# Kernel optimization log

Hardware: AMD Instinct MI355X
Metric: run time of the kernel (lower is better)

## Reference

```python
import jax, jax.numpy as jnp
import numpy as np

B, T, DIN, H, DOUT = 256, 512, 128, 256, 64
LEAK = 0.01


def setup_inputs() -> dict:
    key = jax.random.key(0)
    k0, k1, k2, k3, k4, k5, k6 = jax.random.split(key, 7)
    inputs = jax.random.normal(k0, (B, T, DIN), dtype=jnp.float32)
    # original uses torch.rand(...) * sqrt(dim) for initial states
    x0 = jax.random.uniform(k1, (B, DOUT), dtype=jnp.float32) * (DOUT ** 0.5)
    h0 = jax.random.uniform(k2, (B, H), dtype=jnp.float32) * (H ** 0.5)
    # nn.Linear default init scale ~ 1/sqrt(fan_in)
    s1 = (DIN + H) ** -0.5
    s2 = H ** -0.5
    W_ih = jax.random.uniform(k3, (H, DIN + H), dtype=jnp.float32, minval=-s1, maxval=s1)
    b_ih = jax.random.uniform(k4, (H,), dtype=jnp.float32, minval=-s1, maxval=s1)
    W_ho = jax.random.uniform(k5, (DOUT, H), dtype=jnp.float32, minval=-s2, maxval=s2)
    b_ho = jax.random.uniform(k6, (DOUT,), dtype=jnp.float32, minval=-s2, maxval=s2)
    return {"inputs": inputs, "x0": x0, "h0": h0,
            "W_ih": W_ih, "b_ih": b_ih, "W_ho": W_ho, "b_ho": b_ho}


def reference(inputs, x0, h0, W_ih, b_ih, W_ho, b_ho):
    # inputs: [B, T, DIN]; scan over time with hidden state resident.
    def step(h, u_t):  # h: [B,H], u_t: [B,DIN]
        comb = jnp.concatenate([u_t, h], axis=1)           # [B, DIN+H]
        pre = comb @ W_ih.T + b_ih                          # [B, H]
        h_new = jnp.where(pre >= 0, pre, LEAK * pre)        # LeakyReLU(0.01)
        x_t = h_new @ W_ho.T + b_ho                         # [B, DOUT]
        return h_new, (x_t, h_new)

    u_seq = jnp.swapaxes(inputs, 0, 1)                      # [T, B, DIN]
    _, (xs, hs) = jax.lax.scan(step, h0, u_seq)
    # prepend initial states -> [B, T+1, *]
    x = jnp.concatenate([x0[:, None, :], jnp.swapaxes(xs, 0, 1)], axis=1)
    h = jnp.concatenate([h0[:, None, :], jnp.swapaxes(hs, 0, 1)], axis=1)
    return x, h
```

## Files before the change

### kernel.cpp

```cpp
#include <hip/hip_runtime.h>

#define BB 256
#define TT 512
#define DIN 128
#define HH 256
#define DOUT 64
#define X_ELEMS ((long)BB * 513 * DOUT)

typedef short bf16x8 __attribute__((ext_vector_type(8)));
typedef float f32x4 __attribute__((ext_vector_type(4)));
typedef _Float16 half2_t __attribute__((ext_vector_type(2)));
typedef _Float16 half8_t __attribute__((ext_vector_type(8)));

static __device__ inline short f2bf(float f) {
    unsigned u = __float_as_uint(f);
    unsigned r = (u + 0x7FFFu + ((u >> 16) & 1u)) >> 16;
    return (short)r;
}

static __device__ inline float fdot2f(half2_t a, half2_t b, float c) {
#if __has_builtin(__builtin_amdgcn_fdot2)
    return __builtin_amdgcn_fdot2(a, b, c, false);
#else
    return c + (float)a[0] * (float)b[0] + (float)a[1] * (float)b[1];
#endif
}

static __device__ inline float quad_bfly_add(float x) {
    int t = __builtin_amdgcn_mov_dpp(__float_as_int(x), 0xB1, 0xF, 0xF, true);
    x += __int_as_float(t);
    t = __builtin_amdgcn_mov_dpp(__float_as_int(x), 0x4E, 0xF, 0xF, true);
    x += __int_as_float(t);
    return x;
}

#define SA 136
__global__ __launch_bounds__(256) void gemm_u(
        const float* __restrict__ inp, const float* __restrict__ W_ih,
        const float* __restrict__ b_ih, float* __restrict__ out_h) {
    __shared__ __align__(16) short lA[64 * SA];
    __shared__ __align__(16) short lB[64 * SA];
    const int tid = threadIdx.x;
    const int wave = tid >> 6, lane = tid & 63;
    const int quad = lane >> 4, l16 = lane & 15;
    const int m0 = blockIdx.x * 64;
    const int n0 = blockIdx.y * 64;
    const int sm = tid >> 2, skg = tid & 3;
    const int sn = tid & 63, bkg = tid >> 6;

    float4 a4[8], b4[8];
#pragma unroll
    for (int c = 0; c < 4; ++c) {
        const float4* ap = (const float4*)(inp + (long)(m0 + sm) * DIN + c * 32 + skg * 8);
        a4[2 * c] = ap[0]; a4[2 * c + 1] = ap[1];
        const float4* bp = (const float4*)(W_ih + (long)(n0 + sn) * 384 + c * 32 + bkg * 8);
        b4[2 * c] = bp[0]; b4[2 * c + 1] = bp[1];
    }
#pragma unroll
    for (int c = 0; c < 4; ++c) {
        bf16x8 av, bv;
        float4 x0 = a4[2 * c], x1 = a4[2 * c + 1];
        av[0] = f2bf(x0.x); av[1] = f2bf(x0.y); av[2] = f2bf(x0.z); av[3] = f2bf(x0.w);
        av[4] = f2bf(x1.x); av[5] = f2bf(x1.y); av[6] = f2bf(x1.z); av[7] = f2bf(x1.w);
        float4 y0 = b4[2 * c], y1 = b4[2 * c + 1];
        bv[0] = f2bf(y0.x); bv[1] = f2bf(y0.y); bv[2] = f2bf(y0.z); bv[3] = f2bf(y0.w);
        bv[4] = f2bf(y1.x); bv[5] = f2bf(y1.y); bv[6] = f2bf(y1.z); bv[7] = f2bf(y1.w);
        *(bf16x8*)&lA[sm * SA + c * 32 + skg * 8] = av;
        *(bf16x8*)&lB[sn * SA + c * 32 + bkg * 8] = bv;
    }
    __syncthreads();

    f32x4 acc[4];
#pragma unroll
    for (int i = 0; i < 4; i++) acc[i] = (f32x4){0.f, 0.f, 0.f, 0.f};
#pragma unroll
    for (int c = 0; c < 4; ++c) {
        bf16x8 af = *(const bf16x8*)&lA[(wave * 16 + l16) * SA + c * 32 + quad * 8];
#pragma unroll
        for (int nt = 0; nt < 4; ++nt) {
            bf16x8 bf = *(const bf16x8*)&lB[(nt * 16 + l16) * SA + c * 32 + quad * 8];
            acc[nt] = __builtin_amdgcn_mfma_f32_16x16x32_bf16(af, bf, acc[nt], 0, 0, 0);
        }
    }
#pragma unroll
    for (int nt = 0; nt < 4; ++nt) {
#pragma unroll
        for (int r = 0; r < 4; ++r) {
            int m = m0 + wave * 16 + quad * 4 + r;
            int col = n0 + nt * 16 + l16;
            long orow = (long)(m >> 9) * 513 + (m & 511) + 1;
            out_h[orow * HH + col] = acc[nt][r] + b_ih[col];
        }
    }
}

__global__ __launch_bounds__(256) void rnn_seq(
        const float* __restrict__ x0, const float* __restrict__ h0,
        const float* __restrict__ W_ih,
        float* __restrict__ out_x, float* __restrict__ out_h) {
    __shared__ __align__(16) _Float16 hsh[2][4][72];
    const int b = blockIdx.x;
    const int tid = threadIdx.x;
    const int g = tid >> 2;
    const int q = tid & 3;
    const int jm = (g << 2) + q;

    half2_t w[4][32];
    {
        const float* base = W_ih + 128 + 64 * q;
#pragma unroll
        for (int jp = 0; jp < 4; ++jp) {
            const float* wr = base + (long)(4 * g + jp) * 384;
#pragma unroll
            for (int i = 0; i < 16; ++i) {
                float4 v = *(const float4*)(wr + 4 * i);
                w[jp][2 * i]     = (half2_t){(_Float16)v.x, (_Float16)v.y};
                w[jp][2 * i + 1] = (half2_t){(_Float16)v.z, (_Float16)v.w};
            }
        }
    }

    float* hrow = out_h + (long)b * 513 * HH;
    {
        float hv = h0[(long)b * HH + jm];
        hrow[jm] = hv;
        hsh[0][jm >> 6][jm & 63] = (_Float16)hv;
    }
    if (tid < DOUT) out_x[(long)b * 513 * DOUT + tid] = x0[(long)b * DOUT + tid];
    float u = hrow[HH + jm];
    __syncthreads();

    int cur = 0;
    for (int t = 0; t < TT; ++t) {
        const _Float16* hs = &hsh[cur][q][0];
        float a0 = 0.f, a1 = 0.f, a2 = 0.f, a3 = 0.f;
#pragma unroll
        for (int c = 0; c < 8; ++c) {
            half8_t hv = *(const half8_t*)(hs + 8 * c);
            half2_t p0 = {hv[0], hv[1]}, p1 = {hv[2], hv[3]};
            half2_t p2 = {hv[4], hv[5]}, p3 = {hv[6], hv[7]};
            a0 = fdot2f(p0, w[0][4 * c + 0], a0);
            a0 = fdot2f(p1, w[0][4 * c + 1], a0);
            a0 = fdot2f(p2, w[0][4 * c + 2], a0);
            a0 = fdot2f(p3, w[0][4 * c + 3], a0);
            a1 = fdot2f(p0, w[1][4 * c + 0], a1);
            a1 = fdot2f(p1, w[1][4 * c + 1], a1);
            a1 = fdot2f(p2, w[1][4 * c + 2], a1);
            a1 = fdot2f(p3, w[1][4 * c + 3], a1);
            a2 = fdot2f(p0, w[2][4 * c + 0], a2);
            a2 = fdot2f(p1, w[2][4 * c + 1], a2);
            a2 = fdot2f(p2, w[2][4 * c + 2], a2);
            a2 = fdot2f(p3, w[2][4 * c + 3], a2);
            a3 = fdot2f(p0, w[3][4 * c + 0], a3);
            a3 = fdot2f(p1, w[3][4 * c + 1], a3);
            a3 = fdot2f(p2, w[3][4 * c + 2], a3);
            a3 = fdot2f(p3, w[3][4 * c + 3], a3);
        }
        a0 = quad_bfly_add(a0);
        a1 = quad_bfly_add(a1);
        a2 = quad_bfly_add(a2);
        a3 = quad_bfly_add(a3);
        float s = (q == 0) ? a0 : (q == 1) ? a1 : (q == 2) ? a2 : a3;
        float tot = s + u;
        float hn = tot >= 0.f ? tot : 0.01f * tot;
        int nxt = cur ^ 1;
        hsh[nxt][jm >> 6][jm & 63] = (_Float16)hn;
        hrow[(long)(t + 1) * HH + jm] = hn;
        if (t < TT - 1) u = hrow[(long)(t + 2) * HH + jm];
        __syncthreads();
        cur = nxt;
    }
}

#define SX 264
__global__ __launch_bounds__(256) void gemm_x(
        const float* __restrict__ out_h, const float* __restrict__ W_ho,
        const float* __restrict__ b_ho, float* __restrict__ out_x) {
    __shared__ __align__(16) short lA[64 * SX];
    __shared__ __align__(16) short lB[64 * SX];
    const int tid = threadIdx.x;
    const int wave = tid >> 6, lane = tid & 63;
    const int quad = lane >> 4, l16 = lane & 15;
    const int m0 = blockIdx.x * 64;
    const int bb = m0 >> 9, t0 = m0 & 511;
    const float* hsrc = out_h + ((long)bb * 513 + 1 + t0) * HH;
    float* xdst = out_x + ((long)bb * 513 + 1 + t0) * DOUT;
    const int sm = tid >> 2, skg = tid & 3;
    const int sn = tid & 63, bkg = tid >> 6;

#pragma unroll
    for (int ph = 0; ph < 2; ++ph) {
        float4 a4[8], b4[8];
#pragma unroll
        for (int c = 0; c < 4; ++c) {
            int k0 = ph * 128 + c * 32;
            const float4* ap = (const float4*)(hsrc + (long)sm * HH + k0 + skg * 8);
            a4[2 * c] = ap[0]; a4[2 * c + 1] = ap[1];
            const float4* bp = (const float4*)(W_ho + (long)sn * HH + k0 + bkg * 8);
            b4[2 * c] = bp[0]; b4[2 * c + 1] = bp[1];
        }
#pragma unroll
        for (int c = 0; c < 4; ++c) {
            int k0 = ph * 128 + c * 32;
            bf16x8 av, bv;
            float4 x0 = a4[2 * c], x1 = a4[2 * c + 1];
            av[0] = f2bf(x0.x); av[1] = f2bf(x0.y); av[2] = f2bf(x0.z); av[3] = f2bf(x0.w);
            av[4] = f2bf(x1.x); av[5] = f2bf(x1.y); av[6] = f2bf(x1.z); av[7] = f2bf(x1.w);
            float4 y0 = b4[2 * c], y1 = b4[2 * c + 1];
            bv[0] = f2bf(y0.x); bv[1] = f2bf(y0.y); bv[2] = f2bf(y0.z); bv[3] = f2bf(y0.w);
            bv[4] = f2bf(y1.x); bv[5] = f2bf(y1.y); bv[6] = f2bf(y1.z); bv[7] = f2bf(y1.w);
            *(bf16x8*)&lA[sm * SX + k0 + skg * 8] = av;
            *(bf16x8*)&lB[sn * SX + k0 + bkg * 8] = bv;
        }
    }
    __syncthreads();

    f32x4 acc[4];
#pragma unroll
    for (int i = 0; i < 4; i++) acc[i] = (f32x4){0.f, 0.f, 0.f, 0.f};
#pragma unroll
    for (int c = 0; c < 8; ++c) {
        bf16x8 af = *(const bf16x8*)&lA[(wave * 16 + l16) * SX + c * 32 + quad * 8];
#pragma unroll
        for (int nt = 0; nt < 4; ++nt) {
            bf16x8 bf = *(const bf16x8*)&lB[(nt * 16 + l16) * SX + c * 32 + quad * 8];
            acc[nt] = __builtin_amdgcn_mfma_f32_16x16x32_bf16(af, bf, acc[nt], 0, 0, 0);
        }
    }
#pragma unroll
    for (int nt = 0; nt < 4; ++nt) {
#pragma unroll
        for (int r = 0; r < 4; ++r) {
            int mr = wave * 16 + quad * 4 + r;
            int col = nt * 16 + l16;
            xdst[(long)mr * DOUT + col] = acc[nt][r] + b_ho[col];
        }
    }
}

extern "C" void kernel_launch(void* const* d_in, const int* in_sizes, int n_in,
                              void* d_out, int out_size, void* d_ws, size_t ws_size,
                              hipStream_t stream) {
    const float* inp  = (const float*)d_in[0];
    const float* x0   = (const float*)d_in[1];
    const float* h0   = (const float*)d_in[2];
    const float* W_ih = (const float*)d_in[3];
    const float* b_ih = (const float*)d_in[4];
    const float* W_ho = (const float*)d_in[5];
    const float* b_ho = (const float*)d_in[6];
    float* out_x = (float*)d_out;
    float* out_h = out_x + X_ELEMS;

    gemm_u<<<dim3(2048, 4), 256, 0, stream>>>(inp, W_ih, b_ih, out_h);
    rnn_seq<<<dim3(256), 256, 0, stream>>>(x0, h0, W_ih, out_x, out_h);
    gemm_x<<<dim3(2048), 256, 0, stream>>>(out_h, W_ho, b_ho, out_x);
}
```

Measured before the change: 519.1 us.

## Fuse input projection and output projection into single recurrent kernel

Replaces the three-kernel pipeline (MFMA input GEMM, sequential RNN, MFMA output GEMM) with one per-batch recurrent kernel. Each step now also computes the input projection from an fp16 double-buffered input row held in LDS, and the output projection with per-thread W_ho weights kept in registers. This removes two launches and the write-then-read round trip of the precomputed pre-activations through out_h. In exchange the serial critical path gains roughly 50% more dot-product work plus the output dot per step, and register pressure rises sharply (launch_bounds 256,1).

```diff
diff --git a/kernel.cpp b/kernel.cpp
--- a/kernel.cpp
+++ b/kernel.cpp
@@ -7,16 +7,8 @@
 #define DOUT 64
 #define X_ELEMS ((long)BB * 513 * DOUT)
 
-typedef short bf16x8 __attribute__((ext_vector_type(8)));
-typedef float f32x4 __attribute__((ext_vector_type(4)));
 typedef _Float16 half2_t __attribute__((ext_vector_type(2)));
 typedef _Float16 half8_t __attribute__((ext_vector_type(8)));
-
-static __device__ inline short f2bf(float f) {
-    unsigned u = __float_as_uint(f);
-    unsigned r = (u + 0x7FFFu + ((u >> 16) & 1u)) >> 16;
-    return (short)r;
-}
 
 static __device__ inline float fdot2f(half2_t a, half2_t b, float c) {
 #if __has_builtin(__builtin_amdgcn_fdot2)
@@ -34,207 +26,170 @@
     return x;
 }
 
-#define SA 136
-__global__ __launch_bounds__(256) void gemm_u(
-        const float* __restrict__ inp, const float* __restrict__ W_ih,
-        const float* __restrict__ b_ih, float* __restrict__ out_h) {
-    __shared__ __align__(16) short lA[64 * SA];
-    __shared__ __align__(16) short lB[64 * SA];
-    const int tid = threadIdx.x;
-    const int wave = tid >> 6, lane = tid & 63;
-    const int quad = lane >> 4, l16 = lane & 15;
-    const int m0 = blockIdx.x * 64;
-    const int n0 = blockIdx.y * 64;
-    const int sm = tid >> 2, skg = tid & 3;
-    const int sn = tid & 63, bkg = tid >> 6;
-
-    float4 a4[8], b4[8];
-#pragma unroll
-    for (int c = 0; c < 4; ++c) {
-        const float4* ap = (const float4*)(inp + (long)(m0 + sm) * DIN + c * 32 + skg * 8);
-        a4[2 * c] = ap[0]; a4[2 * c + 1] = ap[1];
-        const float4* bp = (const float4*)(W_ih + (long)(n0 + sn) * 384 + c * 32 + bkg * 8);
-        b4[2 * c] = bp[0]; b4[2 * c + 1] = bp[1];
-    }
-#pragma unroll
-    for (int c = 0; c < 4; ++c) {
-        bf16x8 av, bv;
-        float4 x0 = a4[2 * c], x1 = a4[2 * c + 1];
-        av[0] = f2bf(x0.x); av[1] = f2bf(x0.y); av[2] = f2bf(x0.z); av[3] = f2bf(x0.w);
-        av[4] = f2bf(x1.x); av[5] = f2bf(x1.y); av[6] = f2bf(x1.z); av[7] = f2bf(x1.w);
-        float4 y0 = b4[2 * c], y1 = b4[2 * c + 1];
-        bv[0] = f2bf(y0.x); bv[1] = f2bf(y0.y); bv[2] = f2bf(y0.z); bv[3] = f2bf(y0.w);
-        bv[4] = f2bf(y1.x); bv[5] = f2bf(y1.y); bv[6] = f2bf(y1.z); bv[7] = f2bf(y1.w);
-        *(bf16x8*)&lA[sm * SA + c * 32 + skg * 8] = av;
-        *(bf16x8*)&lB[sn * SA + c * 32 + bkg * 8] = bv;
-    }
-    __syncthreads();
-
-    f32x4 acc[4];
-#pragma unroll
-    for (int i = 0; i < 4; i++) acc[i] = (f32x4){0.f, 0.f, 0.f, 0.f};
-#pragma unroll
-    for (int c = 0; c < 4; ++c) {
-        bf16x8 af = *(const bf16x8*)&lA[(wave * 16 + l16) * SA + c * 32 + quad * 8];
-#pragma unroll
-        for (int nt = 0; nt < 4; ++nt) {
-            bf16x8 bf = *(const bf16x8*)&lB[(nt * 16 + l16) * SA + c * 32 + quad * 8];
-            acc[nt] = __builtin_amdgcn_mfma_f32_16x16x32_bf16(af, bf, acc[nt], 0, 0, 0);
-        }
-    }
-#pragma unroll
-    for (int nt = 0; nt < 4; ++nt) {
-#pragma unroll
-        for (int r = 0; r < 4; ++r) {
-            int m = m0 + wave * 16 + quad * 4 + r;
-            int col = n0 + nt * 16 + l16;
-            long orow = (long)(m >> 9) * 513 + (m & 511) + 1;
-            out_h[orow * HH + col] = acc[nt][r] + b_ih[col];
-        }
-    }
-}
-
-__global__ __launch_bounds__(256) void rnn_seq(
-        const float* __restrict__ x0, const float* __restrict__ h0,
-        const float* __restrict__ W_ih,
+__global__ __launch_bounds__(256, 1) void rnn_fused(
+        const float* __restrict__ inp, const float* __restrict__ x0,
+        const float* __restrict__ h0, const float* __restrict__ W_ih,
+        const float* __restrict__ b_ih, const float* __restrict__ W_ho,
+        const float* __restrict__ b_ho,
         float* __restrict__ out_x, float* __restrict__ out_h) {
     __shared__ __align__(16) _Float16 hsh[2][4][72];
+    __shared__ __align__(16) _Float16 ibuf[2][DIN];
     const int b = blockIdx.x;
     const int tid = threadIdx.x;
-    const int g = tid >> 2;
-    const int q = tid & 3;
-    const int jm = (g << 2) + q;
-
-    half2_t w[4][32];
+    const int g = tid >> 2, q = tid & 3;
+    const int jm = tid;
+
+    half2_t wh[4][32];
+    half2_t wu[4][16];
+    half2_t wo[32];
+#pragma unroll
+    for (int jp = 0; jp < 4; ++jp) {
+        const float* wr = W_ih + (long)(4 * g + jp) * 384;
+#pragma unroll
+        for (int i = 0; i < 16; ++i) {
+            float4 v = *(const float4*)(wr + 128 + 64 * q + 4 * i);
+            wh[jp][2 * i]     = (half2_t){(_Float16)v.x, (_Float16)v.y};
+            wh[jp][2 * i + 1] = (half2_t){(_Float16)v.z, (_Float16)v.w};
+        }
+#pragma unroll
+        for (int i = 0; i < 8; ++i) {
+            float4 v = *(const float4*)(wr + 32 * q + 4 * i);
+            wu[jp][2 * i]     = (half2_t){(_Float16)v.x, (_Float16)v.y};
+            wu[jp][2 * i + 1] = (half2_t){(_Float16)v.z, (_Float16)v.w};
+        }
+    }
+#pragma unroll
+    for (int i = 0; i < 16; ++i) {
+        float4 v = *(const float4*)(W_ho + (long)g * HH + 64 * q + 4 * i);
+        wo[2 * i]     = (half2_t){(_Float16)v.x, (_Float16)v.y};
+        wo[2 * i + 1] = (half2_t){(_Float16)v.z, (_Float16)v.w};
+    }
+    const float bih_r = b_ih[jm];
+    const float bho_r = b_ho[g];
+
+    float* hrow = out_h + (long)b * 513 * HH;
+    float* xrow = out_x + (long)b * 513 * DOUT;
+    const float* irow = inp + (long)b * TT * DIN;
+
     {
-        const float* base = W_ih + 128 + 64 * q;
-#pragma unroll
-        for (int jp = 0; jp < 4; ++jp) {
-            const float* wr = base + (long)(4 * g + jp) * 384;
-#pragma unroll
-            for (int i = 0; i < 16; ++i) {
-                float4 v = *(const float4*)(wr + 4 * i);
-                w[jp][2 * i]     = (half2_t){(_Float16)v.x, (_Float16)v.y};
-                w[jp][2 * i + 1] = (half2_t){(_Float16)v.z, (_Float16)v.w};
-            }
-        }
-    }
-
-    float* hrow = out_h + (long)b * 513 * HH;
+        float hv0 = h0[(long)b * HH + jm];
+        hrow[jm] = hv0;
+        hsh[0][tid >> 6][tid & 63] = (_Float16)hv0;
+    }
+    if (tid < DOUT) xrow[tid] = x0[(long)b * DOUT + tid];
+    float2 ipf = {0.f, 0.f};
+    if (tid < 64) {
+        float2 v = *(const float2*)(irow + 2 * tid);
+        *(half2_t*)&ibuf[0][2 * tid] = (half2_t){(_Float16)v.x, (_Float16)v.y};
+        ipf = *(const float2*)(irow + DIN + 2 * tid);
+    }
+    __syncthreads();
+
+    half8_t hv[8];
     {
-        float hv = h0[(long)b * HH + jm];
-        hrow[jm] = hv;
-        hsh[0][jm >> 6][jm & 63] = (_Float16)hv;
-    }
-    if (tid < DOUT) out_x[(long)b * 513 * DOUT + tid] = x0[(long)b * DOUT + tid];
-    float u = hrow[HH + jm];
-    __syncthreads();
-
+        const _Float16* hs = &hsh[0][q][0];
+#pragma unroll
+        for (int c = 0; c < 8; ++c) hv[c] = *(const half8_t*)(hs + 8 * c);
+    }
+
+    const float* ipsrc = irow + 2 * DIN + 2 * tid;
+    float* hst = hrow + HH + jm;
+    float* xst = xrow + DOUT + g;
     int cur = 0;
     for (int t = 0; t < TT; ++t) {
-        const _Float16* hs = &hsh[cur][q][0];
+        float2 ipn = {0.f, 0.f};
+        if (tid < 64 && t < TT - 2) ipn = *(const float2*)ipsrc;
+        ipsrc += DIN;
+
+        const _Float16* ib = &ibuf[t & 1][q * 32];
+        half8_t uv0 = *(const half8_t*)(ib);
+        half8_t uv1 = *(const half8_t*)(ib + 8);
+        half8_t uv2 = *(const half8_t*)(ib + 16);
+        half8_t uv3 = *(const half8_t*)(ib + 24);
+
         float a0 = 0.f, a1 = 0.f, a2 = 0.f, a3 = 0.f;
 #pragma unroll
         for (int c = 0; c < 8; ++c) {
-            half8_t hv = *(const half8_t*)(hs + 8 * c);
-            half2_t p0 = {hv[0], hv[1]}, p1 = {hv[2], hv[3]};
-            half2_t p2 = {hv[4], hv[5]}, p3 = {hv[6], hv[7]};
-            a0 = fdot2f(p0, w[0][4 * c + 0], a0);
-            a0 = fdot2f(p1, w[0][4 * c + 1], a0);
-            a0 = fdot2f(p2, w[0][4 * c + 2], a0);
-            a0 = fdot2f(p3, w[0][4 * c + 3], a0);
-            a1 = fdot2f(p0, w[1][4 * c + 0], a1);
-            a1 = fdot2f(p1, w[1][4 * c + 1], a1);
-            a1 = fdot2f(p2, w[1][4 * c + 2], a1);
-            a1 = fdot2f(p3, w[1][4 * c + 3], a1);
-            a2 = fdot2f(p0, w[2][4 * c + 0], a2);
-            a2 = fdot2f(p1, w[2][4 * c + 1], a2);
-            a2 = fdot2f(p2, w[2][4 * c + 2], a2);
-            a2 = fdot2f(p3, w[2][4 * c + 3], a2);
-            a3 = fdot2f(p0, w[3][4 * c + 0], a3);
-            a3 = fdot2f(p1, w[3][4 * c + 1], a3);
-            a3 = fdot2f(p2, w[3][4 * c + 2], a3);
-            a3 = fdot2f(p3, w[3][4 * c + 3], a3);
-        }
+            half8_t hvv = hv[c];
+            half2_t p0 = {hvv[0], hvv[1]}, p1 = {hvv[2], hvv[3]};
+            half2_t p2 = {hvv[4], hvv[5]}, p3 = {hvv[6], hvv[7]};
+            a0 = fdot2f(p0, wh[0][4 * c + 0], a0);
+            a0 = fdot2f(p1, wh[0][4 * c + 1], a0);
+            a0 = fdot2f(p2, wh[0][4 * c + 2], a0);
+            a0 = fdot2f(p3, wh[0][4 * c + 3], a0);
+            a1 = fdot2f(p0, wh[1][4 * c + 0], a1);
+            a1 = fdot2f(p1, wh[1][4 * c + 1], a1);
+            a1 = fdot2f(p2, wh[1][4 * c + 2], a1);
+            a1 = fdot2f(p3, wh[1][4 * c + 3], a1);
+            a2 = fdot2f(p0, wh[2][4 * c + 0], a2);
+            a2 = fdot2f(p1, wh[2][4 * c + 1], a2);
+            a2 = fdot2f(p2, wh[2][4 * c + 2], a2);
+            a2 = fdot2f(p3, wh[2][4 * c + 3], a2);
+            a3 = fdot2f(p0, wh[3][4 * c + 0], a3);
+            a3 = fdot2f(p1, wh[3][4 * c + 1], a3);
+            a3 = fdot2f(p2, wh[3][4 * c + 2], a3);
+            a3 = fdot2f(p3, wh[3][4 * c + 3], a3);
+        }
+#define UDOT4(UV, c0)                                              \
+        {                                                          \
+            half2_t p0 = {UV[0], UV[1]}, p1 = {UV[2], UV[3]};      \
+            half2_t p2 = {UV[4], UV[5]}, p3 = {UV[6], UV[7]};      \
+            a0 = fdot2f(p0, wu[0][c0 + 0], a0);                    \
+            a0 = fdot2f(p1, wu[0][c0 + 1], a0);                    \
+            a0 = fdot2f(p2, wu[0][c0 + 2], a0);                    \
+            a0 = fdot2f(p3, wu[0][c0 + 3], a0);                    \
+            a1 = fdot2f(p0, wu[1][c0 + 0], a1);                    \
+            a1 = fdot2f(p1, wu[1][c0 + 1], a1);                    \
+            a1 = fdot2f(p2, wu[1][c0 + 2], a1);                    \
+            a1 = fdot2f(p3, wu[1][c0 + 3], a1);                    \
+            a2 = fdot2f(p0, wu[2][c0 + 0], a2);                    \
+            a2 = fdot2f(p1, wu[2][c0 + 1], a2);                    \
+            a2 = fdot2f(p2, wu[2][c0 + 2], a2);                    \
+            a2 = fdot2f(p3, wu[2][c0 + 3], a2);                    \
+            a3 = fdot2f(p0, wu[3][c0 + 0], a3);                    \
+            a3 = fdot2f(p1, wu[3][c0 + 1], a3);                    \
+            a3 = fdot2f(p2, wu[3][c0 + 2], a3);                    \
+            a3 = fdot2f(p3, wu[3][c0 + 3], a3);                    \
+        }
+        UDOT4(uv0, 0)
+        UDOT4(uv1, 4)
+        UDOT4(uv2, 8)
+        UDOT4(uv3, 12)
+#undef UDOT4
+
         a0 = quad_bfly_add(a0);
         a1 = quad_bfly_add(a1);
         a2 = quad_bfly_add(a2);
         a3 = quad_bfly_add(a3);
         float s = (q == 0) ? a0 : (q == 1) ? a1 : (q == 2) ? a2 : a3;
-        float tot = s + u;
+        float tot = s + bih_r;
         float hn = tot >= 0.f ? tot : 0.01f * tot;
         int nxt = cur ^ 1;
-        hsh[nxt][jm >> 6][jm & 63] = (_Float16)hn;
-        hrow[(long)(t + 1) * HH + jm] = hn;
-        if (t < TT - 1) u = hrow[(long)(t + 2) * HH + jm];
+        hsh[nxt][tid >> 6][tid & 63] = (_Float16)hn;
+        hst[0] = hn;
+        hst += HH;
+        if (tid < 64 && t < TT - 1)
+            *(half2_t*)&ibuf[(t + 1) & 1][2 * tid] =
+                (half2_t){(_Float16)ipf.x, (_Float16)ipf.y};
+        ipf = ipn;
         __syncthreads();
+
+        const _Float16* hs = &hsh[nxt][q][0];
+#pragma unroll
+        for (int c = 0; c < 8; ++c) hv[c] = *(const half8_t*)(hs + 8 * c);
+        float ax = 0.f;
+#pragma unroll
+        for (int c = 0; c < 8; ++c) {
+            half8_t hvv = hv[c];
+            ax = fdot2f((half2_t){hvv[0], hvv[1]}, wo[4 * c + 0], ax);
+            ax = fdot2f((half2_t){hvv[2], hvv[3]}, wo[4 * c + 1], ax);
+            ax = fdot2f((half2_t){hvv[4], hvv[5]}, wo[4 * c + 2], ax);
+            ax = fdot2f((half2_t){hvv[6], hvv[7]}, wo[4 * c + 3], ax);
+        }
+        ax = quad_bfly_add(ax);
+        if (q == 0) xst[0] = ax + bho_r;
+        xst += DOUT;
         cur = nxt;
-    }
-}
-
-#define SX 264
-__global__ __launch_bounds__(256) void gemm_x(
-        const float* __restrict__ out_h, const float* __restrict__ W_ho,
-        const float* __restrict__ b_ho, float* __restrict__ out_x) {
-    __shared__ __align__(16) short lA[64 * SX];
-    __shared__ __align__(16) short lB[64 * SX];
-    const int tid = threadIdx.x;
-    const int wave = tid >> 6, lane = tid & 63;
-    const int quad = lane >> 4, l16 = lane & 15;
-    const int m0 = blockIdx.x * 64;
-    const int bb = m0 >> 9, t0 = m0 & 511;
-    const float* hsrc = out_h + ((long)bb * 513 + 1 + t0) * HH;
-    float* xdst = out_x + ((long)bb * 513 + 1 + t0) * DOUT;
-    const int sm = tid >> 2, skg = tid & 3;
-    const int sn = tid & 63, bkg = tid >> 6;
-
-#pragma unroll
-    for (int ph = 0; ph < 2; ++ph) {
-        float4 a4[8], b4[8];
-#pragma unroll
-        for (int c = 0; c < 4; ++c) {
-            int k0 = ph * 128 + c * 32;
-            const float4* ap = (const float4*)(hsrc + (long)sm * HH + k0 + skg * 8);
-            a4[2 * c] = ap[0]; a4[2 * c + 1] = ap[1];
-            const float4* bp = (const float4*)(W_ho + (long)sn * HH + k0 + bkg * 8);
-            b4[2 * c] = bp[0]; b4[2 * c + 1] = bp[1];
-        }
-#pragma unroll
-        for (int c = 0; c < 4; ++c) {
-            int k0 = ph * 128 + c * 32;
-            bf16x8 av, bv;
-            float4 x0 = a4[2 * c], x1 = a4[2 * c + 1];
-            av[0] = f2bf(x0.x); av[1] = f2bf(x0.y); av[2] = f2bf(x0.z); av[3] = f2bf(x0.w);
-            av[4] = f2bf(x1.x); av[5] = f2bf(x1.y); av[6] = f2bf(x1.z); av[7] = f2bf(x1.w);
-            float4 y0 = b4[2 * c], y1 = b4[2 * c + 1];
-            bv[0] = f2bf(y0.x); bv[1] = f2bf(y0.y); bv[2] = f2bf(y0.z); bv[3] = f2bf(y0.w);
-            bv[4] = f2bf(y1.x); bv[5] = f2bf(y1.y); bv[6] = f2bf(y1.z); bv[7] = f2bf(y1.w);
-            *(bf16x8*)&lA[sm * SX + k0 + skg * 8] = av;
-            *(bf16x8*)&lB[sn * SX + k0 + bkg * 8] = bv;
-        }
-    }
-    __syncthreads();
-
-    f32x4 acc[4];
-#pragma unroll
-    for (int i = 0; i < 4; i++) acc[i] = (f32x4){0.f, 0.f, 0.f, 0.f};
-#pragma unroll
-    for (int c = 0; c < 8; ++c) {
-        bf16x8 af = *(const bf16x8*)&lA[(wave * 16 + l16) * SX + c * 32 + quad * 8];
-#pragma unroll
-        for (int nt = 0; nt < 4; ++nt) {
-            bf16x8 bf = *(const bf16x8*)&lB[(nt * 16 + l16) * SX + c * 32 + quad * 8];
-            acc[nt] = __builtin_amdgcn_mfma_f32_16x16x32_bf16(af, bf, acc[nt], 0, 0, 0);
-        }
-    }
-#pragma unroll
-    for (int nt = 0; nt < 4; ++nt) {
-#pragma unroll
-        for (int r = 0; r < 4; ++r) {
-            int mr = wave * 16 + quad * 4 + r;
-            int col = nt * 16 + l16;
-            xdst[(long)mr * DOUT + col] = acc[nt][r] + b_ho[col];
-        }
     }
 }
 
@@ -251,7 +206,6 @@
     float* out_x = (float*)d_out;
     float* out_h = out_x + X_ELEMS;
 
-    gemm_u<<<dim3(2048, 4), 256, 0, stream>>>(inp, W_ih, b_ih, out_h);
-    rnn_seq<<<dim3(256), 256, 0, stream>>>(x0, h0, W_ih, out_x, out_h);
-    gemm_x<<<dim3(2048), 256, 0, stream>>>(out_h, W_ho, b_ho, out_x);
-}
+    rnn_fused<<<dim3(256), 256, 0, stream>>>(inp, x0, h0, W_ih, b_ih, W_ho, b_ho,
+                                             out_x, out_h);
+}
```

Measured after the change: 584.0 us. 1.13x slower.

## Fuse input projection into recurrent kernel with 512-thread blocks and full-wave reduction

Applied to the files above, without the earlier changes.

Removes the separate gemm_u pre-pass, so the recurrent kernel computes the input projection itself from fp16-converted inputs staged in shared memory. Each block now has 512 threads and splits the 384-wide dot product across 16 lanes per group, combining partial sums with DPP and ds_swizzle butterflies. This drops the write and re-read of the u projection through global memory and the extra launch, and shortens the per-step dot chain. In exchange every timestep does more ALU work, the inputs are rounded to fp16 instead of bf16 MFMA, and half the threads sit idle in the state update.

```diff
diff --git a/kernel.cpp b/kernel.cpp
--- a/kernel.cpp
+++ b/kernel.cpp
@@ -10,6 +10,7 @@
 typedef short bf16x8 __attribute__((ext_vector_type(8)));
 typedef float f32x4 __attribute__((ext_vector_type(4)));
 typedef _Float16 half2_t __attribute__((ext_vector_type(2)));
+typedef _Float16 half4_t __attribute__((ext_vector_type(4)));
 typedef _Float16 half8_t __attribute__((ext_vector_type(8)));
 
 static __device__ inline short f2bf(float f) {
@@ -26,150 +27,161 @@
 #endif
 }
 
-static __device__ inline float quad_bfly_add(float x) {
-    int t = __builtin_amdgcn_mov_dpp(__float_as_int(x), 0xB1, 0xF, 0xF, true);
-    x += __int_as_float(t);
-    t = __builtin_amdgcn_mov_dpp(__float_as_int(x), 0x4E, 0xF, 0xF, true);
-    x += __int_as_float(t);
-    return x;
-}
-
-#define SA 136
-__global__ __launch_bounds__(256) void gemm_u(
-        const float* __restrict__ inp, const float* __restrict__ W_ih,
-        const float* __restrict__ b_ih, float* __restrict__ out_h) {
-    __shared__ __align__(16) short lA[64 * SA];
-    __shared__ __align__(16) short lB[64 * SA];
-    const int tid = threadIdx.x;
-    const int wave = tid >> 6, lane = tid & 63;
-    const int quad = lane >> 4, l16 = lane & 15;
-    const int m0 = blockIdx.x * 64;
-    const int n0 = blockIdx.y * 64;
-    const int sm = tid >> 2, skg = tid & 3;
-    const int sn = tid & 63, bkg = tid >> 6;
-
-    float4 a4[8], b4[8];
-#pragma unroll
-    for (int c = 0; c < 4; ++c) {
-        const float4* ap = (const float4*)(inp + (long)(m0 + sm) * DIN + c * 32 + skg * 8);
-        a4[2 * c] = ap[0]; a4[2 * c + 1] = ap[1];
-        const float4* bp = (const float4*)(W_ih + (long)(n0 + sn) * 384 + c * 32 + bkg * 8);
-        b4[2 * c] = bp[0]; b4[2 * c + 1] = bp[1];
-    }
-#pragma unroll
-    for (int c = 0; c < 4; ++c) {
-        bf16x8 av, bv;
-        float4 x0 = a4[2 * c], x1 = a4[2 * c + 1];
-        av[0] = f2bf(x0.x); av[1] = f2bf(x0.y); av[2] = f2bf(x0.z); av[3] = f2bf(x0.w);
-        av[4] = f2bf(x1.x); av[5] = f2bf(x1.y); av[6] = f2bf(x1.z); av[7] = f2bf(x1.w);
-        float4 y0 = b4[2 * c], y1 = b4[2 * c + 1];
-        bv[0] = f2bf(y0.x); bv[1] = f2bf(y0.y); bv[2] = f2bf(y0.z); bv[3] = f2bf(y0.w);
-        bv[4] = f2bf(y1.x); bv[5] = f2bf(y1.y); bv[6] = f2bf(y1.z); bv[7] = f2bf(y1.w);
-        *(bf16x8*)&lA[sm * SA + c * 32 + skg * 8] = av;
-        *(bf16x8*)&lB[sn * SA + c * 32 + bkg * 8] = bv;
-    }
-    __syncthreads();
-
-    f32x4 acc[4];
-#pragma unroll
-    for (int i = 0; i < 4; i++) acc[i] = (f32x4){0.f, 0.f, 0.f, 0.f};
-#pragma unroll
-    for (int c = 0; c < 4; ++c) {
-        bf16x8 af = *(const bf16x8*)&lA[(wave * 16 + l16) * SA + c * 32 + quad * 8];
-#pragma unroll
-        for (int nt = 0; nt < 4; ++nt) {
-            bf16x8 bf = *(const bf16x8*)&lB[(nt * 16 + l16) * SA + c * 32 + quad * 8];
-            acc[nt] = __builtin_amdgcn_mfma_f32_16x16x32_bf16(af, bf, acc[nt], 0, 0, 0);
-        }
-    }
-#pragma unroll
-    for (int nt = 0; nt < 4; ++nt) {
-#pragma unroll
-        for (int r = 0; r < 4; ++r) {
-            int m = m0 + wave * 16 + quad * 4 + r;
-            int col = n0 + nt * 16 + l16;
-            long orow = (long)(m >> 9) * 513 + (m & 511) + 1;
-            out_h[orow * HH + col] = acc[nt][r] + b_ih[col];
-        }
-    }
-}
-
-__global__ __launch_bounds__(256) void rnn_seq(
-        const float* __restrict__ x0, const float* __restrict__ h0,
-        const float* __restrict__ W_ih,
+static __device__ inline float dpp_xor1(float x) {
+    return __int_as_float(
+        __builtin_amdgcn_mov_dpp(__float_as_int(x), 0xB1, 0xF, 0xF, true));
+}
+static __device__ inline float dpp_xor2(float x) {
+    return __int_as_float(
+        __builtin_amdgcn_mov_dpp(__float_as_int(x), 0x4E, 0xF, 0xF, true));
+}
+static __device__ inline float swz_xor4(float x) {
+    return __int_as_float(
+        __builtin_amdgcn_ds_swizzle(__float_as_int(x), 0x101F));
+}
+static __device__ inline float swz_xor8(float x) {
+    return __int_as_float(
+        __builtin_amdgcn_ds_swizzle(__float_as_int(x), 0x201F));
+}
+
+__global__ __launch_bounds__(512, 2) void rnn_seq(
+        const float* __restrict__ inp, const float* __restrict__ x0,
+        const float* __restrict__ h0, const float* __restrict__ W_ih,
+        const float* __restrict__ b_ih,
         float* __restrict__ out_x, float* __restrict__ out_h) {
-    __shared__ __align__(16) _Float16 hsh[2][4][72];
+    __shared__ __align__(16) _Float16 hsh[2][16][24];
+    __shared__ __align__(16) _Float16 ibuf[2][16][12];
     const int b = blockIdx.x;
     const int tid = threadIdx.x;
-    const int g = tid >> 2;
-    const int q = tid & 3;
-    const int jm = (g << 2) + q;
-
-    half2_t w[4][32];
-    {
-        const float* base = W_ih + 128 + 64 * q;
-#pragma unroll
-        for (int jp = 0; jp < 4; ++jp) {
-            const float* wr = base + (long)(4 * g + jp) * 384;
-#pragma unroll
-            for (int i = 0; i < 16; ++i) {
-                float4 v = *(const float4*)(wr + 4 * i);
-                w[jp][2 * i]     = (half2_t){(_Float16)v.x, (_Float16)v.y};
-                w[jp][2 * i + 1] = (half2_t){(_Float16)v.z, (_Float16)v.w};
-            }
-        }
-    }
+    const int g = tid >> 4, q = tid & 15;
+    const int j = 8 * g + (q & 7);
+    const bool hwv = (q < 8);
+    const bool iwv = (tid < 64);
+
+    half2_t wh[8][8];
+    half2_t wu[8][4];
+#pragma unroll
+    for (int jp = 0; jp < 8; ++jp) {
+        const float* wr = W_ih + (long)(8 * g + jp) * 384;
+#pragma unroll
+        for (int m = 0; m < 4; ++m) {
+            float4 v = *(const float4*)(wr + 128 + 16 * q + 4 * m);
+            wh[jp][2 * m]     = (half2_t){(_Float16)v.x, (_Float16)v.y};
+            wh[jp][2 * m + 1] = (half2_t){(_Float16)v.z, (_Float16)v.w};
+        }
+#pragma unroll
+        for (int m = 0; m < 2; ++m) {
+            float4 v = *(const float4*)(wr + 8 * q + 4 * m);
+            wu[jp][2 * m]     = (half2_t){(_Float16)v.x, (_Float16)v.y};
+            wu[jp][2 * m + 1] = (half2_t){(_Float16)v.z, (_Float16)v.w};
+        }
+    }
+#pragma unroll
+    for (int jp = 0; jp < 8; ++jp) {
+#pragma unroll
+        for (int i = 0; i < 8; ++i) asm volatile("" : "+v"(wh[jp][i]));
+#pragma unroll
+        for (int i = 0; i < 4; ++i) asm volatile("" : "+v"(wu[jp][i]));
+    }
+    const float bih = b_ih[j];
 
     float* hrow = out_h + (long)b * 513 * HH;
-    {
-        float hv = h0[(long)b * HH + jm];
-        hrow[jm] = hv;
-        hsh[0][jm >> 6][jm & 63] = (_Float16)hv;
-    }
-    if (tid < DOUT) out_x[(long)b * 513 * DOUT + tid] = x0[(long)b * DOUT + tid];
-    float u = hrow[HH + jm];
+    float* xrow = out_x + (long)b * 513 * DOUT;
+    const float* irow = inp + (long)b * TT * DIN;
+
+    float hprev = 0.f;
+    if (hwv) {
+        hprev = h0[(long)b * HH + j];
+        hsh[0][j >> 4][j & 15] = (_Float16)hprev;
+    }
+    if (tid < DOUT) xrow[tid] = x0[(long)b * DOUT + tid];
+    float2 ipf = {0.f, 0.f};
+    if (iwv) {
+        float2 v = *(const float2*)(irow + 2 * tid);
+        *(half2_t*)&ibuf[0][tid >> 2][2 * (tid & 3)] =
+            (half2_t){(_Float16)v.x, (_Float16)v.y};
+        ipf = *(const float2*)(irow + DIN + 2 * tid);
+    }
     __syncthreads();
 
-    int cur = 0;
-    for (int t = 0; t < TT; ++t) {
-        const _Float16* hs = &hsh[cur][q][0];
-        float a0 = 0.f, a1 = 0.f, a2 = 0.f, a3 = 0.f;
-#pragma unroll
-        for (int c = 0; c < 8; ++c) {
-            half8_t hv = *(const half8_t*)(hs + 8 * c);
-            half2_t p0 = {hv[0], hv[1]}, p1 = {hv[2], hv[3]};
-            half2_t p2 = {hv[4], hv[5]}, p3 = {hv[6], hv[7]};
-            a0 = fdot2f(p0, w[0][4 * c + 0], a0);
-            a0 = fdot2f(p1, w[0][4 * c + 1], a0);
-            a0 = fdot2f(p2, w[0][4 * c + 2], a0);
-            a0 = fdot2f(p3, w[0][4 * c + 3], a0);
-            a1 = fdot2f(p0, w[1][4 * c + 0], a1);
-            a1 = fdot2f(p1, w[1][4 * c + 1], a1);
-            a1 = fdot2f(p2, w[1][4 * c + 2], a1);
-            a1 = fdot2f(p3, w[1][4 * c + 3], a1);
-            a2 = fdot2f(p0, w[2][4 * c + 0], a2);
-            a2 = fdot2f(p1, w[2][4 * c + 1], a2);
-            a2 = fdot2f(p2, w[2][4 * c + 2], a2);
-            a2 = fdot2f(p3, w[2][4 * c + 3], a2);
-            a3 = fdot2f(p0, w[3][4 * c + 0], a3);
-            a3 = fdot2f(p1, w[3][4 * c + 1], a3);
-            a3 = fdot2f(p2, w[3][4 * c + 2], a3);
-            a3 = fdot2f(p3, w[3][4 * c + 3], a3);
-        }
-        a0 = quad_bfly_add(a0);
-        a1 = quad_bfly_add(a1);
-        a2 = quad_bfly_add(a2);
-        a3 = quad_bfly_add(a3);
-        float s = (q == 0) ? a0 : (q == 1) ? a1 : (q == 2) ? a2 : a3;
-        float tot = s + u;
-        float hn = tot >= 0.f ? tot : 0.01f * tot;
-        int nxt = cur ^ 1;
-        hsh[nxt][jm >> 6][jm & 63] = (_Float16)hn;
-        hrow[(long)(t + 1) * HH + jm] = hn;
-        if (t < TT - 1) u = hrow[(long)(t + 2) * HH + jm];
-        __syncthreads();
-        cur = nxt;
-    }
+    half8_t hva = *(const half8_t*)&hsh[0][q][0];
+    half8_t hvb = *(const half8_t*)&hsh[0][q][8];
+
+    const float* ipsrc = irow + 2 * DIN + 2 * tid;
+    float* hst = hrow + j;
+
+#define STEP(T, PC, PN)                                                     \
+    {                                                                       \
+                    \
+        if (hwv) hst[0] = hprev;                                            \
+        hst += HH;                                                          \
+                                                  \
+        float2 ipn = {0.f, 0.f};                                            \
+        if (iwv && (T) + 2 < TT) ipn = *(const float2*)ipsrc;               \
+        ipsrc += DIN;                                                       \
+                                             \
+        half4_t uva = *(const half4_t*)&ibuf[PC][q][0];                     \
+        half4_t uvb = *(const half4_t*)&ibuf[PC][q][4];                     \
+        half2_t hp0 = {hva[0], hva[1]}, hp1 = {hva[2], hva[3]};             \
+        half2_t hp2 = {hva[4], hva[5]}, hp3 = {hva[6], hva[7]};             \
+        half2_t hp4 = {hvb[0], hvb[1]}, hp5 = {hvb[2], hvb[3]};             \
+        half2_t hp6 = {hvb[4], hvb[5]}, hp7 = {hvb[6], hvb[7]};             \
+        half2_t up0 = {uva[0], uva[1]}, up1 = {uva[2], uva[3]};             \
+        half2_t up2 = {uvb[0], uvb[1]}, up3 = {uvb[2], uvb[3]};             \
+        float r[8];                                                         \
+        _Pragma("unroll")                                                   \
+        for (int jp = 0; jp < 8; ++jp) {                                    \
+            float a = 0.f;                                                  \
+            a = fdot2f(hp0, wh[jp][0], a);                                  \
+            a = fdot2f(hp1, wh[jp][1], a);                                  \
+            a = fdot2f(hp2, wh[jp][2], a);                                  \
+            a = fdot2f(hp3, wh[jp][3], a);                                  \
+            a = fdot2f(hp4, wh[jp][4], a);                                  \
+            a = fdot2f(hp5, wh[jp][5], a);                                  \
+            a = fdot2f(hp6, wh[jp][6], a);                                  \
+            a = fdot2f(hp7, wh[jp][7], a);                                  \
+            a = fdot2f(up0, wu[jp][0], a);                                  \
+            a = fdot2f(up1, wu[jp][1], a);                                  \
+            a = fdot2f(up2, wu[jp][2], a);                                  \
+            a = fdot2f(up3, wu[jp][3], a);                                  \
+            r[jp] = a;                                                      \
+        }                                                                   \
+            \
+        float s, k;                                                         \
+        s = (q & 1) ? r[0] : r[1]; k = (q & 1) ? r[1] : r[0];               \
+        float n0 = k + dpp_xor1(s);                                         \
+        s = (q & 1) ? r[2] : r[3]; k = (q & 1) ? r[3] : r[2];               \
+        float n1 = k + dpp_xor1(s);                                         \
+        s = (q & 1) ? r[4] : r[5]; k = (q & 1) ? r[5] : r[4];               \
+        float n2 = k + dpp_xor1(s);                                         \
+        s = (q & 1) ? r[6] : r[7]; k = (q & 1) ? r[7] : r[6];               \
+        float n3 = k + dpp_xor1(s);                                         \
+        s = (q & 2) ? n0 : n1; k = (q & 2) ? n1 : n0;                       \
+        float m0 = k + dpp_xor2(s);                                         \
+        s = (q & 2) ? n2 : n3; k = (q & 2) ? n3 : n2;                       \
+        float m1 = k + dpp_xor2(s);                                         \
+        s = (q & 4) ? m0 : m1; k = (q & 4) ? m1 : m0;                       \
+        float v8 = k + swz_xor4(s);                                         \
+        float sum = v8 + swz_xor8(v8);                                      \
+        float tot = sum + bih;                                              \
+        float hn = tot >= 0.f ? tot : 0.01f * tot;           \
+        if (hwv) hsh[PN][j >> 4][j & 15] = (_Float16)hn;                    \
+        if (iwv) *(half2_t*)&ibuf[PN][tid >> 2][2 * (tid & 3)] =            \
+            (half2_t){(_Float16)ipf.x, (_Float16)ipf.y};                    \
+        ipf = ipn;                                                          \
+        hprev = hn;                                                         \
+        __syncthreads();                                                    \
+                                   \
+        hva = *(const half8_t*)&hsh[PN][q][0];                              \
+        hvb = *(const half8_t*)&hsh[PN][q][8];                              \
+    }
+
+    for (int t = 0; t < TT; t += 2) {
+        STEP(t,     0, 1)
+        STEP(t + 1, 1, 0)
+    }
+    if (hwv) hst[0] = hprev;
+#undef STEP
 }
 
 #define SX 264
@@ -203,9 +215,9 @@
         for (int c = 0; c < 4; ++c) {
             int k0 = ph * 128 + c * 32;
             bf16x8 av, bv;
-            float4 x0 = a4[2 * c], x1 = a4[2 * c + 1];
-            av[0] = f2bf(x0.x); av[1] = f2bf(x0.y); av[2] = f2bf(x0.z); av[3] = f2bf(x0.w);
-            av[4] = f2bf(x1.x); av[5] = f2bf(x1.y); av[6] = f2bf(x1.z); av[7] = f2bf(x1.w);
+            float4 x0v = a4[2 * c], x1v = a4[2 * c + 1];
+            av[0] = f2bf(x0v.x); av[1] = f2bf(x0v.y); av[2] = f2bf(x0v.z); av[3] = f2bf(x0v.w);
+            av[4] = f2bf(x1v.x); av[5] = f2bf(x1v.y); av[6] = f2bf(x1v.z); av[7] = f2bf(x1v.w);
             float4 y0 = b4[2 * c], y1 = b4[2 * c + 1];
             bv[0] = f2bf(y0.x); bv[1] = f2bf(y0.y); bv[2] = f2bf(y0.z); bv[3] = f2bf(y0.w);
             bv[4] = f2bf(y1.x); bv[5] = f2bf(y1.y); bv[6] = f2bf(y1.z); bv[7] = f2bf(y1.w);
@@ -251,7 +263,6 @@
     float* out_x = (float*)d_out;
     float* out_h = out_x + X_ELEMS;
 
-    gemm_u<<<dim3(2048, 4), 256, 0, stream>>>(inp, W_ih, b_ih, out_h);
-    rnn_seq<<<dim3(256), 256, 0, stream>>>(x0, h0, W_ih, out_x, out_h);
+    rnn_seq<<<dim3(256), 512, 0, stream>>>(inp, x0, h0, W_ih, b_ih, out_x, out_h);
     gemm_x<<<dim3(2048), 256, 0, stream>>>(out_h, W_ho, b_ho, out_x);
 }
```

Result: slower. 547.4 us (+5.5%).
